# Performance work log

Hardware: AMD Instinct MI355X
Metric: run time of the kernel (lower is better)

## Reference

```python
import jax, jax.numpy as jnp
import numpy as np

SUB1 = 0.5
SUB2 = 0.2


def setup_inputs() -> dict:
    key = jax.random.key(0)
    k1, k2, k3 = jax.random.split(key, 3)
    x = jax.random.normal(k1, (32, 64, 128, 128), dtype=jnp.float32)
    conv_weight = jax.random.normal(k2, (128, 64, 3, 3), dtype=jnp.float32) * 0.05
    conv_bias = jax.random.normal(k3, (128,), dtype=jnp.float32) * 0.05
    return {"x": x, "conv_weight": conv_weight, "conv_bias": conv_bias}


def reference(x, conv_weight, conv_bias):
    # Conv2d, stride 1, VALID padding (kernel computes out_h = in_h - K + 1)
    y = jax.lax.conv_general_dilated(
        x, conv_weight,
        window_strides=(1, 1), padding="VALID",
        dimension_numbers=("NCHW", "OIHW", "NCHW"))
    y = y + conv_bias[None, :, None, None]
    v = y - SUB1 - SUB2
    # Mish: v * tanh(softplus(v)); softplus == log(1 + exp(v)) (stable form)
    return v * jnp.tanh(jax.nn.softplus(v))
```

## Files before the change

kernel.cpp:

```cpp
#include <hip/hip_runtime.h>
#include <hip/hip_bf16.h>

typedef short bf16x8 __attribute__((ext_vector_type(8)));
typedef float f32x4 __attribute__((ext_vector_type(4)));

constexpr int C_IN = 64, H_IN = 128, W_IN = 128, C_OUT = 128, OH = 126, OW = 126;
constexpr int PAD = 72;
constexpr float SUBC = 0.7f;

constexpr size_t WR_BYTES = (size_t)9 * C_OUT * C_IN * 2;
constexpr size_t XB_BYTES = (size_t)32 * H_IN * W_IN * C_IN * 2;

__device__ __forceinline__ void gl_lds16(const void* g, void* l) {
    __builtin_amdgcn_global_load_lds(
        (const __attribute__((address_space(1))) unsigned int*)g,
        (__attribute__((address_space(3))) unsigned int*)l, 16, 0, 0);
}

__global__ void reorder_weights(const float* __restrict__ w, __hip_bfloat16* __restrict__ wr) {
    int o = blockIdx.x * 256 + threadIdx.x;
    if (o >= 9 * C_OUT * C_IN) return;
    int ci = o & 63;
    int co = (o >> 6) & 127;
    int k9 = o >> 13;
    int kh = k9 / 3, kw = k9 % 3;
    int cb = ci >> 3, e = ci & 7;
    int dst = (k9 << 13) + (co << 6) + (((cb ^ co) & 7) << 3) + e;
    wr[dst] = __float2bfloat16(w[((co * C_IN + ci) * 3 + kh) * 3 + kw]);
}

__global__ __launch_bounds__(256) void convert_x(const float* __restrict__ x, __hip_bfloat16* __restrict__ xb) {
    int b   = blockIdx.x;
    int tid = threadIdx.x;
    const float* src = x + (size_t)(b >> 7) * (C_IN * H_IN * W_IN) + (size_t)(b & 127) * W_IN;
    __hip_bfloat16* dst = xb + (size_t)b * (W_IN * C_IN);
    for (int r = 0; r < 4; ++r) {
        int t  = tid + r * 256;
        int cb = t & 7;
        int w  = t >> 3;
        alignas(16) __hip_bfloat16 tmp[8];
        #pragma unroll
        for (int e = 0; e < 8; ++e)
            tmp[e] = __float2bfloat16(src[(size_t)(cb * 8 + e) * (H_IN * W_IN) + w]);
        *(bf16x8*)&dst[(w << 6) + (((cb ^ w) & 7) << 3)] = *(const bf16x8*)tmp;
    }
}

__global__ __launch_bounds__(256, 2) void conv_mish_pipe(
    const __hip_bfloat16* __restrict__ xb, const __hip_bfloat16* __restrict__ wr,
    const float* __restrict__ bias, float* __restrict__ out)
{
    __shared__ alignas(16) __hip_bfloat16 smem[4 * 8192];

    int b  = blockIdx.x;
    int lb = (b & 7) * 504 + (b >> 3);
    int n  = lb / OH;
    int oh = lb % OH;

    int tid  = threadIdx.x;
    int lane = tid & 63;
    int wv   = tid >> 6;
    int wm   = wv >> 1;
    int wn   = wv & 1;
    int quad = lane >> 4;
    int l16  = lane & 15;

    f32x4 acc[4][4] = {};

    const __hip_bfloat16* xbase = xb + ((size_t)n * H_IN + oh) * (W_IN * C_IN);

    auto stage = [&](const __hip_bfloat16* src, __hip_bfloat16* dst) {
        const char* s = (const char*)src + (wv << 12) + (lane << 4);
        char* d = (char*)dst + (wv << 12);
        #pragma unroll
        for (int r = 0; r < 4; ++r)
            gl_lds16(s + r * 1024, d + r * 1024);
    };

    stage(xbase, smem);
    stage(wr, smem + 2 * 8192);
    __syncthreads();

    for (int s = 0; s < 9; ++s) {
        int kh = s / 3, kw = s - kh * 3;
        int p = s & 1, q = kh & 1;
        if (s < 8) stage(wr + (size_t)(s + 1) * 8192, smem + (2 + (p ^ 1)) * 8192);
        if (kw == 0 && kh < 2) stage(xbase + (size_t)(kh + 1) * (W_IN * C_IN), smem + (q ^ 1) * 8192);

        const __hip_bfloat16* Xp = smem + q * 8192;
        const __hip_bfloat16* Bp = smem + (2 + p) * 8192;
        #pragma unroll
        for (int half = 0; half < 2; ++half) {
            int g = half * 4 + quad;
            bf16x8 a[4], bfr[4];
            #pragma unroll
            for (int j = 0; j < 4; ++j) {
                int co = wn * 64 + j * 16 + l16;
                bfr[j] = *(const bf16x8*)&Bp[(co << 6) + (((g ^ co) & 7) << 3)];
            }
            #pragma unroll
            for (int i = 0; i < 4; ++i) {
                int m = wm * 64 + i * 16 + l16 + kw;
                int widx = m > 127 ? 127 : m;
                a[i] = *(const bf16x8*)&Xp[(widx << 6) + (((g ^ widx) & 7) << 3)];
            }
            #pragma unroll
            for (int i = 0; i < 4; ++i)
                #pragma unroll
                for (int j = 0; j < 4; ++j)
                    acc[i][j] = __builtin_amdgcn_mfma_f32_16x16x32_bf16(a[i], bfr[j], acc[i][j], 0, 0, 0);
        }
        if (s < 8) __syncthreads();
    }

    for (int j = 0; j < 4; ++j) {
        int co = wn * 64 + j * 16 + l16;
        float bb = bias[co] - SUBC;
        for (int i = 0; i < 4; ++i) {
            int ow0 = wm * 64 + i * 16 + quad * 4;
            float o[4];
            for (int r = 0; r < 4; ++r) {
                float v = acc[i][j][r] + bb;
                float e = __expf(v);
                float t = e * (e + 2.0f);
                float m = v * t * __builtin_amdgcn_rcpf(t + 2.0f);
                o[r] = (v > 20.0f) ? v : m;
            }
            float* dst = out + (((size_t)n * C_OUT + co) * OH + oh) * OW + ow0;
            float2 p0; p0.x = o[0]; p0.y = o[1];
            *(float2*)dst = p0;
            if (ow0 + 2 < OW) {
                float2 p1; p1.x = o[2]; p1.y = o[3];
                *(float2*)(dst + 2) = p1;
            }
        }
    }
}

__global__ __launch_bounds__(256, 2) void conv_mish_legacy(
    const float* __restrict__ x, const __hip_bfloat16* __restrict__ wr,
    const float* __restrict__ bias, float* __restrict__ out)
{
    __shared__ __hip_bfloat16 Xs[128 * PAD];
    __shared__ __hip_bfloat16 Bs[128 * PAD];

    int b = blockIdx.x;
    int lb = (b & 7) * 504 + (b >> 3);
    int n  = lb / OH;
    int oh = lb % OH;

    int tid  = threadIdx.x;
    int lane = tid & 63;
    int wv   = tid >> 6;
    int wm   = wv >> 1;
    int wn   = wv & 1;
    int quad = lane >> 4;
    int l16  = lane & 15;

    f32x4 acc[4][4] = {};
    const float* xn = x + (size_t)n * C_IN * H_IN * W_IN;

    for (int kh = 0; kh < 3; ++kh) {
        __syncthreads();
        {
            int h = oh + kh;
            for (int r = 0; r < 4; ++r) {
                int t  = tid + r * 256;
                int w  = t & 127;
                int cb = t >> 7;
                const float* gp = xn + ((size_t)(cb * 8) * H_IN + h) * W_IN + w;
                alignas(16) __hip_bfloat16 tmp[8];
                #pragma unroll
                for (int e = 0; e < 8; ++e)
                    tmp[e] = __float2bfloat16(gp[(size_t)e * (H_IN * W_IN)]);
                *(bf16x8*)&Xs[w * PAD + cb * 8] = *(const bf16x8*)tmp;
            }
        }
        {
            const __hip_bfloat16* src = wr + ((kh * 3 + 0) << 13);
            for (int r = 0; r < 4; ++r) {
                int c   = tid + r * 256;
                int co  = c >> 3;
                int ci8 = (c & 7) << 3;
                *(bf16x8*)&Bs[co * PAD + ci8] = *(const bf16x8*)(src + co * 64 + ci8);
            }
        }
        __syncthreads();

        for (int kw = 0; kw < 3; ++kw) {
            if (kw) {
                __syncthreads();
                const __hip_bfloat16* src = wr + ((kh * 3 + kw) << 13);
                for (int r = 0; r < 4; ++r) {
                    int c   = tid + r * 256;
                    int co  = c >> 3;
                    int ci8 = (c & 7) << 3;
                    *(bf16x8*)&Bs[co * PAD + ci8] = *(const bf16x8*)(src + co * 64 + ci8);
                }
                __syncthreads();
            }
            #pragma unroll
            for (int half = 0; half < 2; ++half) {
                int k0 = half * 32 + quad * 8;
                int g  = half * 4 + quad;
                bf16x8 a[4], bfr[4];
                #pragma unroll
                for (int j = 0; j < 4; ++j) {
                    int co = wn * 64 + j * 16 + l16;
                    bfr[j] = *(const bf16x8*)&Bs[co * PAD + (((g ^ co) & 7) << 3)];
                }
                #pragma unroll
                for (int i = 0; i < 4; ++i) {
                    int m = wm * 64 + i * 16 + l16;
                    int widx = m + kw; if (widx > 127) widx = 127;
                    a[i] = *(const bf16x8*)&Xs[widx * PAD + k0];
                }
                #pragma unroll
                for (int i = 0; i < 4; ++i)
                    #pragma unroll
                    for (int j = 0; j < 4; ++j)
                        acc[i][j] = __builtin_amdgcn_mfma_f32_16x16x32_bf16(a[i], bfr[j], acc[i][j], 0, 0, 0);
            }
        }
    }

    for (int j = 0; j < 4; ++j) {
        int co = wn * 64 + j * 16 + l16;
        float bb = bias[co] - SUBC;
        for (int i = 0; i < 4; ++i) {
            int ow0 = wm * 64 + i * 16 + quad * 4;
            float o[4];
            for (int r = 0; r < 4; ++r) {
                float v = acc[i][j][r] + bb;
                float e = __expf(v);
                float t = e * (e + 2.0f);
                float m = v * t * __builtin_amdgcn_rcpf(t + 2.0f);
                o[r] = (v > 20.0f) ? v : m;
            }
            float* dst = out + (((size_t)n * C_OUT + co) * OH + oh) * OW + ow0;
            float2 p0; p0.x = o[0]; p0.y = o[1];
            *(float2*)dst = p0;
            if (ow0 + 2 < OW) {
                float2 p1; p1.x = o[2]; p1.y = o[3];
                *(float2*)(dst + 2) = p1;
            }
        }
    }
}

extern "C" void kernel_launch(void* const* d_in, const int* in_sizes, int n_in,
                              void* d_out, int out_size, void* d_ws, size_t ws_size,
                              hipStream_t stream) {
    const float* x    = (const float*)d_in[0];
    const float* w    = (const float*)d_in[1];
    const float* bias = (const float*)d_in[2];
    float* out        = (float*)d_out;
    __hip_bfloat16* wr = (__hip_bfloat16*)d_ws;

    reorder_weights<<<(9 * C_OUT * C_IN + 255) / 256, 256, 0, stream>>>(w, wr);

    if (ws_size >= WR_BYTES + XB_BYTES) {
        __hip_bfloat16* xb = (__hip_bfloat16*)((char*)d_ws + WR_BYTES);
        convert_x<<<32 * H_IN, 256, 0, stream>>>(x, xb);
        conv_mish_pipe<<<32 * OH, 256, 0, stream>>>(xb, wr, bias, out);
    } else {
        conv_mish_legacy<<<32 * OH, 256, 0, stream>>>(x, wr, bias, out);
    }
}
```

Before: 450.5 us.

## Compute two output rows per block to reuse weight tiles across rows

Each block now computes two adjacent output rows instead of one. It keeps three input rows in a rotating LDS ring and loads each weight slice once for both rows, which halves the weight traffic and the barrier count per output row. The cost is doubled accumulator registers (128 floats per thread) and more LDS (80KB), which may lower occupancy or cause spills under the 2-blocks-per-CU launch bound. The grid halves to 2016 blocks.

```diff
diff --git a/kernel.cpp b/kernel.cpp
--- a/kernel.cpp
+++ b/kernel.cpp
@@ -46,16 +46,16 @@
     }
 }
 
-__global__ __launch_bounds__(256, 2) void conv_mish_pipe(
+__global__ __launch_bounds__(256, 2) void conv_mish_pair(
     const __hip_bfloat16* __restrict__ xb, const __hip_bfloat16* __restrict__ wr,
     const float* __restrict__ bias, float* __restrict__ out)
 {
-    __shared__ alignas(16) __hip_bfloat16 smem[4 * 8192];
+    __shared__ alignas(16) __hip_bfloat16 smem[5 * 8192];
 
     int b  = blockIdx.x;
-    int lb = (b & 7) * 504 + (b >> 3);
-    int n  = lb / OH;
-    int oh = lb % OH;
+    int lb = (b & 7) * 252 + (b >> 3);
+    int n  = lb / 63;
+    int oh0 = (lb % 63) * 2;
 
     int tid  = threadIdx.x;
     int lane = tid & 63;
@@ -65,9 +65,9 @@
     int quad = lane >> 4;
     int l16  = lane & 15;
 
-    f32x4 acc[4][4] = {};
-
-    const __hip_bfloat16* xbase = xb + ((size_t)n * H_IN + oh) * (W_IN * C_IN);
+    f32x4 acc[2][4][4] = {};
+
+    const __hip_bfloat16* xbase = xb + ((size_t)n * H_IN + oh0) * (W_IN * C_IN);
 
     auto stage = [&](const __hip_bfloat16* src, __hip_bfloat16* dst) {
         const char* s = (const char*)src + (wv << 12) + (lane << 4);
@@ -77,40 +77,163 @@
             gl_lds16(s + r * 1024, d + r * 1024);
     };
 
-    stage(xbase, smem);
-    stage(wr, smem + 2 * 8192);
+    stage(xbase,            smem);
+    stage(xbase + 8192,     smem + 8192);
+    stage(wr,               smem + 3 * 8192);
     __syncthreads();
 
-    for (int s = 0; s < 9; ++s) {
-        int kh = s / 3, kw = s - kh * 3;
-        int p = s & 1, q = kh & 1;
-        if (s < 8) stage(wr + (size_t)(s + 1) * 8192, smem + (2 + (p ^ 1)) * 8192);
-        if (kw == 0 && kh < 2) stage(xbase + (size_t)(kh + 1) * (W_IN * C_IN), smem + (q ^ 1) * 8192);
-
-        const __hip_bfloat16* Xp = smem + q * 8192;
-        const __hip_bfloat16* Bp = smem + (2 + p) * 8192;
+    #pragma unroll
+    for (int kh = 0; kh < 3; ++kh) {
         #pragma unroll
-        for (int half = 0; half < 2; ++half) {
-            int g = half * 4 + quad;
-            bf16x8 a[4], bfr[4];
+        for (int kw = 0; kw < 3; ++kw) {
+            const int s = kh * 3 + kw;
+            if (s < 8) stage(wr + (size_t)(s + 1) * 8192, smem + (3 + ((s + 1) & 1)) * 8192);
+            if (kw == 0 && kh < 2) stage(xbase + (size_t)(kh + 2) * 8192, smem + ((kh + 2) % 3) * 8192);
+
+            const __hip_bfloat16* Xa = smem + (kh % 3) * 8192;
+            const __hip_bfloat16* Xc = smem + ((kh + 1) % 3) * 8192;
+            const __hip_bfloat16* Bp = smem + (3 + (s & 1)) * 8192;
             #pragma unroll
-            for (int j = 0; j < 4; ++j) {
-                int co = wn * 64 + j * 16 + l16;
-                bfr[j] = *(const bf16x8*)&Bp[(co << 6) + (((g ^ co) & 7) << 3)];
+            for (int half = 0; half < 2; ++half) {
+                int g = half * 4 + quad;
+                bf16x8 bfr[4], a0[4], a1[4];
+                #pragma unroll
+                for (int j = 0; j < 4; ++j) {
+                    int co = wn * 64 + j * 16 + l16;
+                    bfr[j] = *(const bf16x8*)&Bp[(co << 6) + (((g ^ co) & 7) << 3)];
+                }
+                #pragma unroll
+                for (int i = 0; i < 4; ++i) {
+                    int m = wm * 64 + i * 16 + l16 + kw;
+                    int widx = m > 127 ? 127 : m;
+                    int off = (widx << 6) + (((g ^ widx) & 7) << 3);
+                    a0[i] = *(const bf16x8*)&Xa[off];
+                    a1[i] = *(const bf16x8*)&Xc[off];
+                }
+                #pragma unroll
+                for (int i = 0; i < 4; ++i)
+                    #pragma unroll
+                    for (int j = 0; j < 4; ++j) {
+                        acc[0][i][j] = __builtin_amdgcn_mfma_f32_16x16x32_bf16(a0[i], bfr[j], acc[0][i][j], 0, 0, 0);
+                        acc[1][i][j] = __builtin_amdgcn_mfma_f32_16x16x32_bf16(a1[i], bfr[j], acc[1][i][j], 0, 0, 0);
+                    }
+            }
+            if (s < 8) __syncthreads();
+        }
+    }
+
+    #pragma unroll
+    for (int r2 = 0; r2 < 2; ++r2) {
+        for (int j = 0; j < 4; ++j) {
+            int co = wn * 64 + j * 16 + l16;
+            float bb = bias[co] - SUBC;
+            for (int i = 0; i < 4; ++i) {
+                int ow0 = wm * 64 + i * 16 + quad * 4;
+                float o[4];
+                for (int r = 0; r < 4; ++r) {
+                    float v = acc[r2][i][j][r] + bb;
+                    float e = __expf(v);
+                    float t = e * (e + 2.0f);
+                    float m = v * t * __builtin_amdgcn_rcpf(t + 2.0f);
+                    o[r] = (v > 20.0f) ? v : m;
+                }
+                float* dst = out + (((size_t)n * C_OUT + co) * OH + (oh0 + r2)) * OW + ow0;
+                float2 p0; p0.x = o[0]; p0.y = o[1];
+                *(float2*)dst = p0;
+                if (ow0 + 2 < OW) {
+                    float2 p1; p1.x = o[2]; p1.y = o[3];
+                    *(float2*)(dst + 2) = p1;
+                }
+            }
+        }
+    }
+}
+
+__global__ __launch_bounds__(256, 2) void conv_mish_legacy(
+    const float* __restrict__ x, const __hip_bfloat16* __restrict__ wr,
+    const float* __restrict__ bias, float* __restrict__ out)
+{
+    __shared__ __hip_bfloat16 Xs[128 * PAD];
+    __shared__ __hip_bfloat16 Bs[128 * PAD];
+
+    int b = blockIdx.x;
+    int lb = (b & 7) * 504 + (b >> 3);
+    int n  = lb / OH;
+    int oh = lb % OH;
+
+    int tid  = threadIdx.x;
+    int lane = tid & 63;
+    int wv   = tid >> 6;
+    int wm   = wv >> 1;
+    int wn   = wv & 1;
+    int quad = lane >> 4;
+    int l16  = lane & 15;
+
+    f32x4 acc[4][4] = {};
+    const float* xn = x + (size_t)n * C_IN * H_IN * W_IN;
+
+    for (int kh = 0; kh < 3; ++kh) {
+        __syncthreads();
+        {
+            int h = oh + kh;
+            for (int r = 0; r < 4; ++r) {
+                int t  = tid + r * 256;
+                int w  = t & 127;
+                int cb = t >> 7;
+                const float* gp = xn + ((size_t)(cb * 8) * H_IN + h) * W_IN + w;
+                alignas(16) __hip_bfloat16 tmp[8];
+                #pragma unroll
+                for (int e = 0; e < 8; ++e)
+                    tmp[e] = __float2bfloat16(gp[(size_t)e * (H_IN * W_IN)]);
+                *(bf16x8*)&Xs[w * PAD + cb * 8] = *(const bf16x8*)tmp;
+            }
+        }
+        {
+            const __hip_bfloat16* src = wr + ((kh * 3 + 0) << 13);
+            for (int r = 0; r < 4; ++r) {
+                int c   = tid + r * 256;
+                int co  = c >> 3;
+                int ci8 = (c & 7) << 3;
+                *(bf16x8*)&Bs[co * PAD + ci8] = *(const bf16x8*)(src + co * 64 + ci8);
+            }
+        }
+        __syncthreads();
+
+        for (int kw = 0; kw < 3; ++kw) {
+            if (kw) {
+                __syncthreads();
+                const __hip_bfloat16* src = wr + ((kh * 3 + kw) << 13);
+                for (int r = 0; r < 4; ++r) {
+                    int c   = tid + r * 256;
+                    int co  = c >> 3;
+                    int ci8 = (c & 7) << 3;
+                    *(bf16x8*)&Bs[co * PAD + ci8] = *(const bf16x8*)(src + co * 64 + ci8);
+                }
+                __syncthreads();
             }
             #pragma unroll
-            for (int i = 0; i < 4; ++i) {
-                int m = wm * 64 + i * 16 + l16 + kw;
-                int widx = m > 127 ? 127 : m;
-                a[i] = *(const bf16x8*)&Xp[(widx << 6) + (((g ^ widx) & 7) << 3)];
-            }
-            #pragma unroll
-            for (int i = 0; i < 4; ++i)
-                #pragma unroll
-                for (int j = 0; j < 4; ++j)
-                    acc[i][j] = __builtin_amdgcn_mfma_f32_16x16x32_bf16(a[i], bfr[j], acc[i][j], 0, 0, 0);
-        }
-        if (s < 8) __syncthreads();
+            for (int half = 0; half < 2; ++half) {
+                int k0 = half * 32 + quad * 8;
+                int g  = half * 4 + quad;
+                bf16x8 a[4], bfr[4];
+                #pragma unroll
+                for (int j = 0; j < 4; ++j) {
+                    int co = wn * 64 + j * 16 + l16;
+                    bfr[j] = *(const bf16x8*)&Bs[co * PAD + (((g ^ co) & 7) << 3)];
+                }
+                #pragma unroll
+                for (int i = 0; i < 4; ++i) {
+                    int m = wm * 64 + i * 16 + l16;
+                    int widx = m + kw; if (widx > 127) widx = 127;
+                    a[i] = *(const bf16x8*)&Xs[widx * PAD + k0];
+                }
+                #pragma unroll
+                for (int i = 0; i < 4; ++i)
+                    #pragma unroll
+                    for (int j = 0; j < 4; ++j)
+                        acc[i][j] = __builtin_amdgcn_mfma_f32_16x16x32_bf16(a[i], bfr[j], acc[i][j], 0, 0, 0);
+            }
+        }
     }
 
     for (int j = 0; j < 4; ++j) {
@@ -137,117 +260,6 @@
     }
 }
 
-__global__ __launch_bounds__(256, 2) void conv_mish_legacy(
-    const float* __restrict__ x, const __hip_bfloat16* __restrict__ wr,
-    const float* __restrict__ bias, float* __restrict__ out)
-{
-    __shared__ __hip_bfloat16 Xs[128 * PAD];
-    __shared__ __hip_bfloat16 Bs[128 * PAD];
-
-    int b = blockIdx.x;
-    int lb = (b & 7) * 504 + (b >> 3);
-    int n  = lb / OH;
-    int oh = lb % OH;
-
-    int tid  = threadIdx.x;
-    int lane = tid & 63;
-    int wv   = tid >> 6;
-    int wm   = wv >> 1;
-    int wn   = wv & 1;
-    int quad = lane >> 4;
-    int l16  = lane & 15;
-
-    f32x4 acc[4][4] = {};
-    const float* xn = x + (size_t)n * C_IN * H_IN * W_IN;
-
-    for (int kh = 0; kh < 3; ++kh) {
-        __syncthreads();
-        {
-            int h = oh + kh;
-            for (int r = 0; r < 4; ++r) {
-                int t  = tid + r * 256;
-                int w  = t & 127;
-                int cb = t >> 7;
-                const float* gp = xn + ((size_t)(cb * 8) * H_IN + h) * W_IN + w;
-                alignas(16) __hip_bfloat16 tmp[8];
-                #pragma unroll
-                for (int e = 0; e < 8; ++e)
-                    tmp[e] = __float2bfloat16(gp[(size_t)e * (H_IN * W_IN)]);
-                *(bf16x8*)&Xs[w * PAD + cb * 8] = *(const bf16x8*)tmp;
-            }
-        }
-        {
-            const __hip_bfloat16* src = wr + ((kh * 3 + 0) << 13);
-            for (int r = 0; r < 4; ++r) {
-                int c   = tid + r * 256;
-                int co  = c >> 3;
-                int ci8 = (c & 7) << 3;
-                *(bf16x8*)&Bs[co * PAD + ci8] = *(const bf16x8*)(src + co * 64 + ci8);
-            }
-        }
-        __syncthreads();
-
-        for (int kw = 0; kw < 3; ++kw) {
-            if (kw) {
-                __syncthreads();
-                const __hip_bfloat16* src = wr + ((kh * 3 + kw) << 13);
-                for (int r = 0; r < 4; ++r) {
-                    int c   = tid + r * 256;
-                    int co  = c >> 3;
-                    int ci8 = (c & 7) << 3;
-                    *(bf16x8*)&Bs[co * PAD + ci8] = *(const bf16x8*)(src + co * 64 + ci8);
-                }
-                __syncthreads();
-            }
-            #pragma unroll
-            for (int half = 0; half < 2; ++half) {
-                int k0 = half * 32 + quad * 8;
-                int g  = half * 4 + quad;
-                bf16x8 a[4], bfr[4];
-                #pragma unroll
-                for (int j = 0; j < 4; ++j) {
-                    int co = wn * 64 + j * 16 + l16;
-                    bfr[j] = *(const bf16x8*)&Bs[co * PAD + (((g ^ co) & 7) << 3)];
-                }
-                #pragma unroll
-                for (int i = 0; i < 4; ++i) {
-                    int m = wm * 64 + i * 16 + l16;
-                    int widx = m + kw; if (widx > 127) widx = 127;
-                    a[i] = *(const bf16x8*)&Xs[widx * PAD + k0];
-                }
-                #pragma unroll
-                for (int i = 0; i < 4; ++i)
-                    #pragma unroll
-                    for (int j = 0; j < 4; ++j)
-                        acc[i][j] = __builtin_amdgcn_mfma_f32_16x16x32_bf16(a[i], bfr[j], acc[i][j], 0, 0, 0);
-            }
-        }
-    }
-
-    for (int j = 0; j < 4; ++j) {
-        int co = wn * 64 + j * 16 + l16;
-        float bb = bias[co] - SUBC;
-        for (int i = 0; i < 4; ++i) {
-            int ow0 = wm * 64 + i * 16 + quad * 4;
-            float o[4];
-            for (int r = 0; r < 4; ++r) {
-                float v = acc[i][j][r] + bb;
-                float e = __expf(v);
-                float t = e * (e + 2.0f);
-                float m = v * t * __builtin_amdgcn_rcpf(t + 2.0f);
-                o[r] = (v > 20.0f) ? v : m;
-            }
-            float* dst = out + (((size_t)n * C_OUT + co) * OH + oh) * OW + ow0;
-            float2 p0; p0.x = o[0]; p0.y = o[1];
-            *(float2*)dst = p0;
-            if (ow0 + 2 < OW) {
-                float2 p1; p1.x = o[2]; p1.y = o[3];
-                *(float2*)(dst + 2) = p1;
-            }
-        }
-    }
-}
-
 extern "C" void kernel_launch(void* const* d_in, const int* in_sizes, int n_in,
                               void* d_out, int out_size, void* d_ws, size_t ws_size,
                               hipStream_t stream) {
@@ -262,7 +274,7 @@
     if (ws_size >= WR_BYTES + XB_BYTES) {
         __hip_bfloat16* xb = (__hip_bfloat16*)((char*)d_ws + WR_BYTES);
         convert_x<<<32 * H_IN, 256, 0, stream>>>(x, xb);
-        conv_mish_pipe<<<32 * OH, 256, 0, stream>>>(xb, wr, bias, out);
+        conv_mish_pair<<<32 * 63, 256, 0, stream>>>(xb, wr, bias, out);
     } else {
         conv_mish_legacy<<<32 * OH, 256, 0, stream>>>(x, wr, bias, out);
     }
```

After: 459.6 us. +2.0%, slower.
